# Performance work log

Hardware: AMD Instinct MI355X
Metric: run time of the kernel (lower is better)

The kernel has to match this reference:

```python
import jax, jax.numpy as jnp
import numpy as np

DIM_IN = 512
DIM_OUT = 64


def setup_inputs() -> dict:
    key = jax.random.key(0)
    kx, kq, kk, kv = jax.random.split(key, 4)
    x = jax.random.normal(kx, (4, 4096, DIM_IN), dtype=jnp.float32)
    s = 1.0 / np.sqrt(DIM_IN)
    # torch nn.Linear stores weight as [out, in]; keep same convention
    Wq = jax.random.uniform(kq, (DIM_OUT, DIM_IN), jnp.float32, -s, s)
    Wk = jax.random.uniform(kk, (DIM_OUT, DIM_IN), jnp.float32, -s, s)
    Wv = jax.random.uniform(kv, (DIM_OUT, DIM_IN), jnp.float32, -s, s)
    return {"x": x, "Wq": Wq, "Wk": Wk, "Wv": Wv}


def reference(x, Wq, Wk, Wv):
    # q/k/v projections: [B,S,Din] @ [Din,Dout] -> [B,S,Dout]
    q = jnp.einsum("bsd,od->bso", x, Wq)
    k = jnp.einsum("bsd,od->bso", x, Wk)
    v = jnp.einsum("bsd,od->bso", x, Wv)
    scale = 1.0 / jnp.sqrt(jnp.asarray(q.shape[-1], q.dtype))
    scores = jnp.einsum("bqo,bko->bqk", q, k) * scale  # [B,S,S]
    weights = jax.nn.softmax(scores, axis=-1)
    out = jnp.einsum("bqk,bko->bqo", weights, v)  # [B,S,Dout]
    return out
```

## Files before the change

### kernel.cpp

```cpp
#include <hip/hip_runtime.h>
#include <hip/hip_bf16.h>

#define SEQ 4096
#define MTOT 16384

typedef float f32x4  __attribute__((ext_vector_type(4)));
typedef float f32x16 __attribute__((ext_vector_type(16)));
typedef _Float16 f16;
typedef _Float16 f16x4 __attribute__((ext_vector_type(4)));
typedef _Float16 f16x8 __attribute__((ext_vector_type(8)));
typedef unsigned int   u32;
typedef unsigned int   u32x2 __attribute__((ext_vector_type(2)));
typedef unsigned short u16;

static constexpr size_t QL_B   = 0;
static constexpr size_t KL_B   = 2u << 20;
static constexpr size_t VL_B   = 4u << 20;
static constexpr size_t WL_B   = 6u << 20;
static constexpr size_t PART_B = 8u << 20;
static constexpr size_t ML_B   = 42u << 20;

__device__ __forceinline__ u16 h16(float v) { return __builtin_bit_cast(u16, (f16)v); }
__device__ __forceinline__ u32 pkrtz(float a, float b) {
  return __builtin_bit_cast(u32, __builtin_amdgcn_cvt_pkrtz(a, b));
}
__device__ __forceinline__ float ex2(float x) { return __builtin_amdgcn_exp2f(x); }
__device__ __forceinline__ void gl16(const u16* g, u16* l) {
  __builtin_amdgcn_global_load_lds((const __attribute__((address_space(1))) void*)g,
                                   (__attribute__((address_space(3))) void*)l, 16, 0, 0);
}

__global__ __launch_bounds__(256) void wconv_kernel(const float* __restrict__ Wq,
                                                    const float* __restrict__ Wk,
                                                    const float* __restrict__ Wv,
                                                    u16* __restrict__ wlin) {
  const float QSC = 0.18033688011112042f;
  int e = blockIdx.x * 256 + threadIdx.x;
  int flat = e * 4;
  int colg = flat >> 9;
  int k0   = flat & 511;
  int mat  = colg >> 6;
  const float* W = (mat == 0) ? Wq : (mat == 1 ? Wk : Wv);
  f32x4 v = *(const f32x4*)(W + (size_t)(colg & 63) * 512 + k0);
  if (mat == 0) v *= QSC;
  int s = colg >> 4, r16 = colg & 15;
  int step = k0 >> 5, g = (k0 & 31) >> 3, jb = k0 & 7;
  __attribute__((aligned(8))) u16 b[4];
#pragma unroll
  for (int j = 0; j < 4; ++j) b[j] = h16(v[j]);
  *(uint2*)(wlin + ((size_t)(s * 16 + step) * 64 + g * 16 + r16) * 8 + jb) = *(uint2*)b;
}

__global__ __launch_bounds__(256, 4) void proj_kernel(const float* __restrict__ x,
                                                      const u16* __restrict__ wlin,
                                                      u16* __restrict__ ws) {
  __shared__ __attribute__((aligned(16))) u16 xl[8192];
  float* scr = (float*)xl;

  const int tid  = threadIdx.x;
  const int blk  = blockIdx.x;
  const int lane = tid & 63;
  const int ng   = tid >> 6;
  const int r16  = lane & 15;
  const int g    = lane >> 4;
  const int m0   = blk * 16;

#pragma unroll
  for (int i = 0; i < 8; ++i) {
    int f = tid * 4 + i * 1024;
    int row = f >> 9, k0 = f & 511;
    f32x4 v = *(const f32x4*)(x + (size_t)m0 * 512 + f);
    __attribute__((aligned(8))) u16 b[4];
#pragma unroll
    for (int j = 0; j < 4; ++j) b[j] = h16(v[j]);
    int ln = ((k0 & 31) >> 3) * 16 + row;
    *(uint2*)(xl + ((size_t)(k0 >> 5) * 64 + ln) * 8 + (k0 & 7)) = *(uint2*)b;
  }
  __syncthreads();

  f32x4 acc[3];
#pragma unroll
  for (int s = 0; s < 3; ++s) acc[s] = (f32x4){0.f, 0.f, 0.f, 0.f};

#pragma unroll 2
  for (int step = 0; step < 16; ++step) {
    f16x8 a = *(const f16x8*)(xl + ((size_t)step * 64 + lane) * 8);
#pragma unroll
    for (int s = 0; s < 3; ++s) {
      int sg = ng * 3 + s;
      f16x8 b = *(const f16x8*)(wlin + ((size_t)(sg * 16 + step) * 64 + lane) * 8);
      acc[s] = __builtin_amdgcn_mfma_f32_16x16x32_f16(a, b, acc[s], 0, 0, 0);
    }
  }
  __syncthreads();

#pragma unroll
  for (int s = 0; s < 3; ++s)
#pragma unroll
    for (int rr = 0; rr < 4; ++rr)
      scr[(g * 4 + rr) * 193 + ng * 48 + s * 16 + r16] = acc[s][rr];
  __syncthreads();

  u16* Ql = ws + (QL_B >> 1);
  u16* Kl = ws + (KL_B >> 1);
  u16* Vl = ws + (VL_B >> 1);
  const int batch = m0 >> 12;
  const int tile  = (m0 >> 5) & 127;
  const int half  = (m0 >> 4) & 1;

  {
    int t2 = tid & 127;
    int r  = t2 & 15, hh = (t2 >> 4) & 1, ch = t2 >> 5;
    int l31 = half * 16 + r;
    __attribute__((aligned(16))) u16 b[8];
    if (tid < 128) {
#pragma unroll
      for (int j = 0; j < 8; ++j) b[j] = h16(scr[r * 193 + 64 + ch * 16 + hh * 8 + j]);
      *(uint4*)(Kl + ((size_t)((batch * 128 + tile) * 4 + ch) * 64 + hh * 32 + l31) * 8) =
          *(uint4*)b;
    } else {
#pragma unroll
      for (int j = 0; j < 8; ++j) b[j] = h16(scr[r * 193 + ch * 16 + hh * 8 + j]);
      int qhalf = (m0 >> 5);
      *(uint4*)(Ql + ((size_t)(qhalf * 4 + ch) * 64 + hh * 32 + l31) * 8) = *(uint4*)b;
    }
  }
  {
    int z = tid & 1, l31 = (tid >> 1) & 31, hh = (tid >> 6) & 1, db = tid >> 7;
    int d = db * 32 + l31;
    __attribute__((aligned(8))) u16 b[4];
#pragma unroll
    for (int j = 0; j < 4; ++j) b[j] = h16(scr[(8 * z + 4 * hh + j) * 193 + 128 + d]);
    *(uint2*)(Vl + ((size_t)(((batch * 128 + tile) * 2 + db) * 2 + half) * 64 + hh * 32 + l31) *
                       8 + z * 4) = *(uint2*)b;
  }
}

__global__ __launch_bounds__(256, 4) void attn_kernel(u16* __restrict__ ws) {
  __shared__ __attribute__((aligned(16))) u16 kvb[2][8192];

  const int tid  = threadIdx.x;
  const int w    = tid >> 6;
  const int lane = tid & 63;
  const int l31  = lane & 31;
  const int h    = lane >> 5;
  const int bx   = blockIdx.x;
  const int qb   = bx >> 3;
  const int sp   = bx & 7;
  const int bb   = qb >> 5;
  const int q0   = qb * 128 + w * 32;

  const u16* Ql = ws + (QL_B >> 1);
  const u16* Kl = ws + (KL_B >> 1);
  const u16* Vl = ws + (VL_B >> 1);

  const int qhalf = qb * 4 + w;
  f16x8 qf[4];
#pragma unroll
  for (int ch = 0; ch < 4; ++ch)
    qf[ch] = *(const f16x8*)(Ql + ((size_t)(qhalf * 4 + ch) * 64 + lane) * 8);

  f32x16 oacc[2];
#pragma unroll
  for (int db = 0; db < 2; ++db)
#pragma unroll
    for (int r = 0; r < 16; ++r) oacc[db][r] = 0.f;
  float mrun = -INFINITY, lrun = 0.f;
  const float RTHR = 11.0f;

  const int kt0 = bb * 128 + sp * 16;

  auto stage = [&](int b, int p) {
#pragma unroll
    for (int cc = 0; cc < 4; ++cc) {
      const int c = w * 4 + cc;
      const u16* src;
      if (c < 8) {
        src = Kl + (size_t)(kt0 + p * 2 + (c >> 2)) * 2048 + (c & 3) * 512 + lane * 8;
      } else {
        const int c2 = c - 8;
        src = Vl + (size_t)(kt0 + p * 2 + (c2 >> 2)) * 2048 + (c2 & 3) * 512 + lane * 8;
      }
      gl16(src, &kvb[b][c * 512]);
    }
  };

  stage(0, 0);
  __syncthreads();

#pragma unroll 1
  for (int p = 0; p < 8; ++p) {
    const int cur = p & 1;
    if (p < 7) stage(cur ^ 1, p + 1);

#pragma unroll
    for (int s = 0; s < 2; ++s) {
      f16x8 ka[4], vp[2][2];
#pragma unroll
      for (int ch = 0; ch < 4; ++ch)
        ka[ch] = *(const f16x8*)&kvb[cur][((s << 2) + ch) * 512 + lane * 8];
#pragma unroll
      for (int db = 0; db < 2; ++db)
#pragma unroll
        for (int pp = 0; pp < 2; ++pp)
          vp[db][pp] = *(const f16x8*)&kvb[cur][(8 + (s << 2) + db * 2 + pp) * 512 + lane * 8];

      f32x16 sac;
#pragma unroll
      for (int r = 0; r < 16; ++r) sac[r] = 0.f;
#pragma unroll
      for (int ch = 0; ch < 4; ++ch)
        sac = __builtin_amdgcn_mfma_f32_32x32x16_f16(ka[ch], qf[ch], sac, 0, 0, 0);

      float mt = sac[0];
#pragma unroll
      for (int r = 1; r < 16; ++r) mt = fmaxf(mt, sac[r]);
      if (__any(mt > mrun + RTHR)) {
        float mtw  = fmaxf(mt, __shfl_xor(mt, 32));
        float nm   = fmaxf(mrun, mtw);
        float corr = ex2(mrun - nm);
        lrun *= corr;
        mrun = nm;
#pragma unroll
        for (int db = 0; db < 2; ++db)
#pragma unroll
          for (int r = 0; r < 16; ++r) oacc[db][r] *= corr;
      }
#pragma unroll
      for (int r = 0; r < 16; ++r) {
        float pv = ex2(sac[r] - mrun);
        sac[r] = pv;
        lrun += pv;
      }

      f16x4 pb[4];
#pragma unroll
      for (int c = 0; c < 4; ++c) {
        u32x2 pk;
        pk[0] = pkrtz(sac[4 * c + 0], sac[4 * c + 1]);
        pk[1] = pkrtz(sac[4 * c + 2], sac[4 * c + 3]);
        pb[c] = __builtin_bit_cast(f16x4, pk);
      }

#pragma unroll
      for (int db = 0; db < 2; ++db)
#pragma unroll
        for (int pp = 0; pp < 2; ++pp) {
          f16x4 vlo = __builtin_shufflevector(vp[db][pp], vp[db][pp], 0, 1, 2, 3);
          f16x4 vhi = __builtin_shufflevector(vp[db][pp], vp[db][pp], 4, 5, 6, 7);
          oacc[db] = __builtin_amdgcn_mfma_f32_32x32x8f16(vlo, pb[2 * pp], oacc[db], 0, 0, 0);
          oacc[db] = __builtin_amdgcn_mfma_f32_32x32x8f16(vhi, pb[2 * pp + 1], oacc[db], 0, 0, 0);
        }
    }
    __syncthreads();
  }

  lrun += __shfl_xor(lrun, 32);

  float* Op = (float*)((char*)ws + PART_B) + (size_t)sp * MTOT * 64;
#pragma unroll
  for (int db = 0; db < 2; ++db)
#pragma unroll
    for (int g = 0; g < 4; ++g) {
      f32x4 v = {oacc[db][4 * g + 0], oacc[db][4 * g + 1],
                 oacc[db][4 * g + 2], oacc[db][4 * g + 3]};
      *(f32x4*)(Op + (size_t)(q0 + l31) * 64 + db * 32 + 8 * g + 4 * h) = v;
    }
  if (h == 0) {
    float* Mm = (float*)((char*)ws + ML_B);
    float* Ll = Mm + 8 * MTOT;
    Mm[(size_t)sp * MTOT + q0 + l31] = mrun;
    Ll[(size_t)sp * MTOT + q0 + l31] = lrun;
  }
}

__global__ __launch_bounds__(256) void merge_kernel(const u16* __restrict__ ws,
                                                    float* __restrict__ out) {
  int gid = blockIdx.x * 256 + threadIdx.x;
  int row = gid >> 2, dg = gid & 3;
  const float* Mm = (const float*)((const char*)ws + ML_B);
  const float* Ll = Mm + 8 * MTOT;
  float mv[8];
  float mg = -INFINITY;
#pragma unroll
  for (int i = 0; i < 8; ++i) {
    mv[i] = Mm[(size_t)i * MTOT + row];
    mg = fmaxf(mg, mv[i]);
  }
  float den = 0.f, wv[8];
#pragma unroll
  for (int i = 0; i < 8; ++i) {
    wv[i] = ex2(mv[i] - mg);
    den += wv[i] * Ll[(size_t)i * MTOT + row];
  }
  f32x4 acc[4];
#pragma unroll
  for (int m = 0; m < 4; ++m) acc[m] = (f32x4){0.f, 0.f, 0.f, 0.f};
  const float* Op = (const float*)((const char*)ws + PART_B);
#pragma unroll
  for (int i = 0; i < 8; ++i)
#pragma unroll
    for (int m = 0; m < 4; ++m) {
      f32x4 t = *(const f32x4*)(Op + ((size_t)i * MTOT + row) * 64 + dg * 16 + m * 4);
      acc[m] += wv[i] * t;
    }
  float inv = 1.f / den;
#pragma unroll
  for (int m = 0; m < 4; ++m) {
    f32x4 r = acc[m] * inv;
    *(f32x4*)(out + (size_t)row * 64 + dg * 16 + m * 4) = r;
  }
}

extern "C" void kernel_launch(void* const* d_in, const int* in_sizes, int n_in,
                              void* d_out, int out_size, void* d_ws, size_t ws_size,
                              hipStream_t stream) {
  const float* x  = (const float*)d_in[0];
  const float* Wq = (const float*)d_in[1];
  const float* Wk = (const float*)d_in[2];
  const float* Wv = (const float*)d_in[3];
  u16* ws = (u16*)d_ws;
  (void)in_sizes; (void)n_in; (void)out_size; (void)ws_size;

  wconv_kernel<<<96, 256, 0, stream>>>(Wq, Wk, Wv, ws + (WL_B >> 1));
  proj_kernel<<<1024, 256, 0, stream>>>(x, ws + (WL_B >> 1), ws);
  attn_kernel<<<1024, 256, 0, stream>>>(ws);
  merge_kernel<<<256, 256, 0, stream>>>(ws, (float*)d_out);
}
```

Baseline: 61.21 us.

## Fuse split-K merge into attention via intra-block wave-level key split

Rather than splitting keys across 8 blocks and merging partial outputs in a separate kernel through global memory, each block now owns one 32-row query tile and its four waves each process a quarter of the keys with private double-buffered LDS staging and vmcnt waits instead of block barriers. The partial results are combined in LDS and written straight to the output, removing the merge kernel and the partial-output round trip. In exchange, each wave now loads its own K/V (no sharing across waves), only 512 blocks launch, and occupancy drops to 2 blocks per CU.

```diff
diff --git a/kernel.cpp b/kernel.cpp
--- a/kernel.cpp
+++ b/kernel.cpp
@@ -17,8 +17,6 @@
 static constexpr size_t KL_B   = 2u << 20;
 static constexpr size_t VL_B   = 4u << 20;
 static constexpr size_t WL_B   = 6u << 20;
-static constexpr size_t PART_B = 8u << 20;
-static constexpr size_t ML_B   = 42u << 20;
 
 __device__ __forceinline__ u16 h16(float v) { return __builtin_bit_cast(u16, (f16)v); }
 __device__ __forceinline__ u32 pkrtz(float a, float b) {
@@ -136,8 +134,9 @@
   }
 }
 
-__global__ __launch_bounds__(256, 4) void attn_kernel(u16* __restrict__ ws) {
-  __shared__ __attribute__((aligned(16))) u16 kvb[2][8192];
+__global__ __launch_bounds__(256, 2) void attn_kernel(const u16* __restrict__ ws,
+                                                      float* __restrict__ out) {
+  __shared__ __attribute__((aligned(16))) u16 kvb[4][2][4096];
 
   const int tid  = threadIdx.x;
   const int w    = tid >> 6;
@@ -145,20 +144,17 @@
   const int l31  = lane & 31;
   const int h    = lane >> 5;
   const int bx   = blockIdx.x;
-  const int qb   = bx >> 3;
-  const int sp   = bx & 7;
-  const int bb   = qb >> 5;
-  const int q0   = qb * 128 + w * 32;
+  const int qb   = (bx & 7) * 64 + (bx >> 3);
+  const int bb   = qb >> 7;
 
   const u16* Ql = ws + (QL_B >> 1);
   const u16* Kl = ws + (KL_B >> 1);
   const u16* Vl = ws + (VL_B >> 1);
 
-  const int qhalf = qb * 4 + w;
   f16x8 qf[4];
 #pragma unroll
   for (int ch = 0; ch < 4; ++ch)
-    qf[ch] = *(const f16x8*)(Ql + ((size_t)(qhalf * 4 + ch) * 64 + lane) * 8);
+    qf[ch] = *(const f16x8*)(Ql + ((size_t)(qb * 4 + ch) * 64 + lane) * 8);
 
   f32x16 oacc[2];
 #pragma unroll
@@ -168,147 +164,132 @@
   float mrun = -INFINITY, lrun = 0.f;
   const float RTHR = 11.0f;
 
-  const int kt0 = bb * 128 + sp * 16;
-
-  auto stage = [&](int b, int p) {
-#pragma unroll
-    for (int cc = 0; cc < 4; ++cc) {
-      const int c = w * 4 + cc;
-      const u16* src;
-      if (c < 8) {
-        src = Kl + (size_t)(kt0 + p * 2 + (c >> 2)) * 2048 + (c & 3) * 512 + lane * 8;
-      } else {
-        const int c2 = c - 8;
-        src = Vl + (size_t)(kt0 + p * 2 + (c2 >> 2)) * 2048 + (c2 & 3) * 512 + lane * 8;
+  const int t0 = bb * 128 + w * 32;
+  u16* b0 = &kvb[w][0][0];
+  u16* b1 = &kvb[w][1][0];
+
+  auto stage = [&](u16* buf, int t) {
+    const u16* ks = Kl + (size_t)t * 2048;
+    const u16* vs = Vl + (size_t)t * 2048;
+#pragma unroll
+    for (int c = 0; c < 4; ++c) gl16(ks + c * 512 + lane * 8, buf + c * 512);
+#pragma unroll
+    for (int c = 0; c < 4; ++c) gl16(vs + c * 512 + lane * 8, buf + 2048 + c * 512);
+  };
+
+  stage(b0, t0);
+
+#pragma unroll 1
+  for (int it = 0; it < 32; ++it) {
+    u16* cb = (it & 1) ? b1 : b0;
+    u16* nb = (it & 1) ? b0 : b1;
+    if (it < 31) {
+      stage(nb, t0 + it + 1);
+      asm volatile("s_waitcnt vmcnt(8)" ::: "memory");
+    } else {
+      asm volatile("s_waitcnt vmcnt(0)" ::: "memory");
+    }
+    __builtin_amdgcn_sched_barrier(0);
+
+    f16x8 ka[4], vp[2][2];
+#pragma unroll
+    for (int ch = 0; ch < 4; ++ch)
+      ka[ch] = *(const f16x8*)(cb + (ch * 64 + lane) * 8);
+#pragma unroll
+    for (int db = 0; db < 2; ++db)
+#pragma unroll
+      for (int pp = 0; pp < 2; ++pp)
+        vp[db][pp] = *(const f16x8*)(cb + 2048 + ((db * 2 + pp) * 64 + lane) * 8);
+
+    f32x16 sac;
+#pragma unroll
+    for (int r = 0; r < 16; ++r) sac[r] = 0.f;
+#pragma unroll
+    for (int ch = 0; ch < 4; ++ch)
+      sac = __builtin_amdgcn_mfma_f32_32x32x16_f16(ka[ch], qf[ch], sac, 0, 0, 0);
+
+    float mt = sac[0];
+#pragma unroll
+    for (int r = 1; r < 16; ++r) mt = fmaxf(mt, sac[r]);
+    if (__any(mt > mrun + RTHR)) {
+      float mtw  = fmaxf(mt, __shfl_xor(mt, 32));
+      float nm   = fmaxf(mrun, mtw);
+      float corr = ex2(mrun - nm);
+      lrun *= corr;
+      mrun = nm;
+#pragma unroll
+      for (int db = 0; db < 2; ++db)
+#pragma unroll
+        for (int r = 0; r < 16; ++r) oacc[db][r] *= corr;
+    }
+#pragma unroll
+    for (int r = 0; r < 16; ++r) {
+      float pv = ex2(sac[r] - mrun);
+      sac[r] = pv;
+      lrun += pv;
+    }
+
+    f16x4 pb[4];
+#pragma unroll
+    for (int c = 0; c < 4; ++c) {
+      u32x2 pk;
+      pk[0] = pkrtz(sac[4 * c + 0], sac[4 * c + 1]);
+      pk[1] = pkrtz(sac[4 * c + 2], sac[4 * c + 3]);
+      pb[c] = __builtin_bit_cast(f16x4, pk);
+    }
+
+#pragma unroll
+    for (int db = 0; db < 2; ++db)
+#pragma unroll
+      for (int pp = 0; pp < 2; ++pp) {
+        f16x4 vlo = __builtin_shufflevector(vp[db][pp], vp[db][pp], 0, 1, 2, 3);
+        f16x4 vhi = __builtin_shufflevector(vp[db][pp], vp[db][pp], 4, 5, 6, 7);
+        oacc[db] = __builtin_amdgcn_mfma_f32_32x32x8f16(vlo, pb[2 * pp], oacc[db], 0, 0, 0);
+        oacc[db] = __builtin_amdgcn_mfma_f32_32x32x8f16(vhi, pb[2 * pp + 1], oacc[db], 0, 0, 0);
       }
-      gl16(src, &kvb[b][c * 512]);
-    }
-  };
-
-  stage(0, 0);
-  __syncthreads();
-
-#pragma unroll 1
-  for (int p = 0; p < 8; ++p) {
-    const int cur = p & 1;
-    if (p < 7) stage(cur ^ 1, p + 1);
-
-#pragma unroll
-    for (int s = 0; s < 2; ++s) {
-      f16x8 ka[4], vp[2][2];
-#pragma unroll
-      for (int ch = 0; ch < 4; ++ch)
-        ka[ch] = *(const f16x8*)&kvb[cur][((s << 2) + ch) * 512 + lane * 8];
-#pragma unroll
-      for (int db = 0; db < 2; ++db)
-#pragma unroll
-        for (int pp = 0; pp < 2; ++pp)
-          vp[db][pp] = *(const f16x8*)&kvb[cur][(8 + (s << 2) + db * 2 + pp) * 512 + lane * 8];
-
-      f32x16 sac;
-#pragma unroll
-      for (int r = 0; r < 16; ++r) sac[r] = 0.f;
-#pragma unroll
-      for (int ch = 0; ch < 4; ++ch)
-        sac = __builtin_amdgcn_mfma_f32_32x32x16_f16(ka[ch], qf[ch], sac, 0, 0, 0);
-
-      float mt = sac[0];
-#pragma unroll
-      for (int r = 1; r < 16; ++r) mt = fmaxf(mt, sac[r]);
-      if (__any(mt > mrun + RTHR)) {
-        float mtw  = fmaxf(mt, __shfl_xor(mt, 32));
-        float nm   = fmaxf(mrun, mtw);
-        float corr = ex2(mrun - nm);
-        lrun *= corr;
-        mrun = nm;
-#pragma unroll
-        for (int db = 0; db < 2; ++db)
-#pragma unroll
-          for (int r = 0; r < 16; ++r) oacc[db][r] *= corr;
-      }
-#pragma unroll
-      for (int r = 0; r < 16; ++r) {
-        float pv = ex2(sac[r] - mrun);
-        sac[r] = pv;
-        lrun += pv;
-      }
-
-      f16x4 pb[4];
-#pragma unroll
-      for (int c = 0; c < 4; ++c) {
-        u32x2 pk;
-        pk[0] = pkrtz(sac[4 * c + 0], sac[4 * c + 1]);
-        pk[1] = pkrtz(sac[4 * c + 2], sac[4 * c + 3]);
-        pb[c] = __builtin_bit_cast(f16x4, pk);
-      }
-
-#pragma unroll
-      for (int db = 0; db < 2; ++db)
-#pragma unroll
-        for (int pp = 0; pp < 2; ++pp) {
-          f16x4 vlo = __builtin_shufflevector(vp[db][pp], vp[db][pp], 0, 1, 2, 3);
-          f16x4 vhi = __builtin_shufflevector(vp[db][pp], vp[db][pp], 4, 5, 6, 7);
-          oacc[db] = __builtin_amdgcn_mfma_f32_32x32x8f16(vlo, pb[2 * pp], oacc[db], 0, 0, 0);
-          oacc[db] = __builtin_amdgcn_mfma_f32_32x32x8f16(vhi, pb[2 * pp + 1], oacc[db], 0, 0, 0);
-        }
-    }
-    __syncthreads();
   }
 
   lrun += __shfl_xor(lrun, 32);
 
-  float* Op = (float*)((char*)ws + PART_B) + (size_t)sp * MTOT * 64;
+  __syncthreads();
+  float* po  = (float*)&kvb[0][0][0];
+  float* mls = (float*)((char*)&kvb[0][0][0] + 35840);
+  if (h == 0) {
+    mls[(w * 32 + l31) * 2 + 0] = mrun;
+    mls[(w * 32 + l31) * 2 + 1] = lrun;
+  }
+  __syncthreads();
+
+  float mg = -INFINITY;
+#pragma unroll
+  for (int ww = 0; ww < 4; ++ww) mg = fmaxf(mg, mls[(ww * 32 + l31) * 2]);
+  float wgt = ex2(mrun - mg);
 #pragma unroll
   for (int db = 0; db < 2; ++db)
 #pragma unroll
     for (int g = 0; g < 4; ++g) {
-      f32x4 v = {oacc[db][4 * g + 0], oacc[db][4 * g + 1],
-                 oacc[db][4 * g + 2], oacc[db][4 * g + 3]};
-      *(f32x4*)(Op + (size_t)(q0 + l31) * 64 + db * 32 + 8 * g + 4 * h) = v;
-    }
-  if (h == 0) {
-    float* Mm = (float*)((char*)ws + ML_B);
-    float* Ll = Mm + 8 * MTOT;
-    Mm[(size_t)sp * MTOT + q0 + l31] = mrun;
-    Ll[(size_t)sp * MTOT + q0 + l31] = lrun;
-  }
-}
-
-__global__ __launch_bounds__(256) void merge_kernel(const u16* __restrict__ ws,
-                                                    float* __restrict__ out) {
-  int gid = blockIdx.x * 256 + threadIdx.x;
-  int row = gid >> 2, dg = gid & 3;
-  const float* Mm = (const float*)((const char*)ws + ML_B);
-  const float* Ll = Mm + 8 * MTOT;
-  float mv[8];
-  float mg = -INFINITY;
-#pragma unroll
-  for (int i = 0; i < 8; ++i) {
-    mv[i] = Mm[(size_t)i * MTOT + row];
-    mg = fmaxf(mg, mv[i]);
-  }
-  float den = 0.f, wv[8];
-#pragma unroll
-  for (int i = 0; i < 8; ++i) {
-    wv[i] = ex2(mv[i] - mg);
-    den += wv[i] * Ll[(size_t)i * MTOT + row];
-  }
-  f32x4 acc[4];
-#pragma unroll
-  for (int m = 0; m < 4; ++m) acc[m] = (f32x4){0.f, 0.f, 0.f, 0.f};
-  const float* Op = (const float*)((const char*)ws + PART_B);
-#pragma unroll
-  for (int i = 0; i < 8; ++i)
-#pragma unroll
-    for (int m = 0; m < 4; ++m) {
-      f32x4 t = *(const f32x4*)(Op + ((size_t)i * MTOT + row) * 64 + dg * 16 + m * 4);
-      acc[m] += wv[i] * t;
-    }
-  float inv = 1.f / den;
-#pragma unroll
-  for (int m = 0; m < 4; ++m) {
-    f32x4 r = acc[m] * inv;
-    *(f32x4*)(out + (size_t)row * 64 + dg * 16 + m * 4) = r;
+      f32x4 v = {oacc[db][4 * g + 0] * wgt, oacc[db][4 * g + 1] * wgt,
+                 oacc[db][4 * g + 2] * wgt, oacc[db][4 * g + 3] * wgt};
+      *(f32x4*)(po + (size_t)(w * 32 + l31) * 68 + db * 32 + 8 * g + 4 * h) = v;
+    }
+  __syncthreads();
+
+#pragma unroll
+  for (int i = 0; i < 2; ++i) {
+    int idx = tid + i * 256;
+    int q = idx >> 4, c4 = (idx & 15) * 4;
+    float m2 = -INFINITY;
+#pragma unroll
+    for (int ww = 0; ww < 4; ++ww) m2 = fmaxf(m2, mls[(ww * 32 + q) * 2]);
+    float l2 = 0.f;
+#pragma unroll
+    for (int ww = 0; ww < 4; ++ww)
+      l2 += mls[(ww * 32 + q) * 2 + 1] * ex2(mls[(ww * 32 + q) * 2] - m2);
+    f32x4 s = (f32x4){0.f, 0.f, 0.f, 0.f};
+#pragma unroll
+    for (int ww = 0; ww < 4; ++ww) s += *(const f32x4*)(po + (size_t)(ww * 32 + q) * 68 + c4);
+    s *= (1.f / l2);
+    *(f32x4*)(out + (size_t)(qb * 32 + q) * 64 + c4) = s;
   }
 }
 
@@ -324,6 +305,5 @@
 
   wconv_kernel<<<96, 256, 0, stream>>>(Wq, Wk, Wv, ws + (WL_B >> 1));
   proj_kernel<<<1024, 256, 0, stream>>>(x, ws + (WL_B >> 1), ws);
-  attn_kernel<<<1024, 256, 0, stream>>>(ws);
-  merge_kernel<<<256, 256, 0, stream>>>(ws, (float*)d_out);
-}
+  attn_kernel<<<512, 256, 0, stream>>>(ws, (float*)d_out);
+}
```

Measured after the change: 55.03 us. 1.11x faster.
